# Kernel tuning notes

Hardware: AMD Instinct MI355X
Metric: run time of the kernel (lower is better)

The kernel has to match this reference:

```python
import jax, jax.numpy as jnp
import numpy as np
from jax import lax

B, P, ENC, H, A, E, V, TC = 64, 196, 2048, 1024, 1024, 512, 10000, 32


def setup_inputs() -> dict:
    key = jax.random.key(0)
    ks = jax.random.split(key, 24)
    s = 0.02
    inp = {
        'enc_out': jax.random.normal(ks[0], (B, P, ENC), jnp.float32),
        'enc_captions': jax.random.randint(ks[1], (B, TC), 0, V),
        'lengths': jax.random.randint(ks[2], (B,), 2, TC + 1).at[0].set(TC),
        'W_enc_att': jax.random.normal(ks[3], (A, ENC)) * s,
        'b_enc_att': jnp.zeros((A,)),
        'W_dec_att': jax.random.normal(ks[4], (A, H)) * s,
        'b_dec_att': jnp.zeros((A,)),
        'W_full': jax.random.normal(ks[5], (1, A)) * s,
        'b_full': jnp.zeros((1,)),
        'emb': jax.random.uniform(ks[6], (V, E), minval=-0.1, maxval=0.1),
        'W_ih': jax.random.normal(ks[7], (4 * H, E + ENC)) * s,
        'b_ih': jnp.zeros((4 * H,)),
        'W_hh': jax.random.normal(ks[8], (4 * H, H)) * s,
        'b_hh': jnp.zeros((4 * H,)),
        'W_init_h': jax.random.normal(ks[9], (H, ENC)) * s,
        'b_init_h': jnp.zeros((H,)),
        'W_init_c': jax.random.normal(ks[10], (H, ENC)) * s,
        'b_init_c': jnp.zeros((H,)),
        'W_beta': jax.random.normal(ks[11], (ENC, H)) * s,
        'b_beta': jnp.zeros((ENC,)),
        'W_fc': jax.random.uniform(ks[12], (V, H), minval=-0.1, maxval=0.1),
        'b_fc': jnp.zeros((V,)),
    }
    return inp


def reference(enc_out, enc_captions, lengths,
              W_enc_att, b_enc_att, W_dec_att, b_dec_att, W_full, b_full,
              emb, W_ih, b_ih, W_hh, b_hh,
              W_init_h, b_init_h, W_init_c, b_init_c,
              W_beta, b_beta, W_fc, b_fc):
    T = enc_captions.shape[1] - 1  # static max decode length (setup forces one full-length row)
    ind = jnp.argsort(-lengths)
    lens = lengths[ind]
    eo = enc_out[ind]              # [B,P,ENC] sorted by length desc
    caps = enc_captions[ind]
    dec_lens = lens - 1
    embs = emb[caps]               # [B,TC,E]

    mean_a = eo.mean(axis=1)
    h0 = mean_a @ W_init_h.T + b_init_h
    c0 = mean_a @ W_init_c.T + b_init_c

    # encoder projection is time-invariant; hoist out of the loop
    enc_att = jnp.einsum('bpe,ae->bpa', eo, W_enc_att) + b_enc_att  # [B,P,A]

    mask_ts = jnp.arange(T)[:, None] < dec_lens[None, :]            # [T,B]
    emb_ts = jnp.swapaxes(embs[:, :T, :], 0, 1)                     # [T,B,E]

    def step(carry, xs):
        h, c = carry
        emb_t, m = xs  # [B,E], [B] bool (active rows = leading batch_size_t)
        # attention
        dec = h @ W_dec_att.T + b_dec_att                            # [B,A]
        a = jax.nn.relu(enc_att + dec[:, None, :]) @ W_full[0] + b_full[0]  # [B,P]
        alpha = jax.nn.softmax(a, axis=1)
        context = jnp.einsum('bpe,bp->be', eo, alpha)                # [B,ENC]
        # gate + LSTM cell (torch gate order: i, f, g, o)
        gate = jax.nn.sigmoid(h @ W_beta.T + b_beta)
        awe = gate * context
        x = jnp.concatenate([emb_t, awe], axis=1)
        gates = x @ W_ih.T + b_ih + h @ W_hh.T + b_hh
        i, f, g, o = jnp.split(gates, 4, axis=1)
        c_new = jax.nn.sigmoid(f) * c + jax.nn.sigmoid(i) * jnp.tanh(g)
        h_new = jax.nn.sigmoid(o) * jnp.tanh(c_new)
        m2 = m[:, None]
        h2 = jnp.where(m2, h_new, h)  # inactive rows keep frozen state
        c2 = jnp.where(m2, c_new, c)
        mf = m2.astype(h.dtype)
        preds = (h_new @ W_fc.T + b_fc) * mf  # dropout = identity (eval)
        return (h2, c2), (preds, alpha * mf)

    (_, _), (preds, alphas) = lax.scan(step, (h0, c0), (emb_ts, mask_ts))
    predictions = jnp.swapaxes(preds, 0, 1)   # [B,T,V]
    alphas = jnp.swapaxes(alphas, 0, 1)       # [B,T,P]
    return predictions, alphas, caps, dec_lens, ind
```

## Files before the change

kernel.cpp:

```cpp
#include <hip/hip_runtime.h>

#define Bn   64
#define Pp   196
#define ENCd 2048
#define Hd   1024
#define Ad   1024
#define Ed   512
#define Vd   10000
#define TCd  32
#define Td   31
#define XHW  3584
#define VPAD 10240
#define KHL  6144

typedef short bf16x8 __attribute__((ext_vector_type(8)));
typedef float f32x4  __attribute__((ext_vector_type(4)));

static __device__ __forceinline__ float bf2f(unsigned short u) {
    unsigned int x = ((unsigned int)u) << 16;
    float f; __builtin_memcpy(&f, &x, 4); return f;
}
static __device__ __forceinline__ unsigned short f2bf(float f) {
    unsigned int x; __builtin_memcpy(&x, &f, 4);
    x += 0x7fffu + ((x >> 16) & 1u);
    return (unsigned short)(x >> 16);
}
static __device__ __forceinline__ float sigf(float x) { return 1.f / (1.f + expf(-x)); }

static __device__ __forceinline__ void gl_lds16(const unsigned short* g, unsigned short* l) {
    __builtin_amdgcn_global_load_lds((const __attribute__((address_space(1))) void*)g,
                                     (__attribute__((address_space(3))) void*)l,
                                     16, 0, 0);
}


__global__ void sort_kernel(const int* __restrict__ lengths, const int* __restrict__ captions,
                            int* __restrict__ ind, int* __restrict__ dl,
                            float* __restrict__ out_caps, float* __restrict__ out_dl,
                            float* __restrict__ out_ind) {
    __shared__ int s_ind[Bn];
    int tid = threadIdx.x;
    int Lt = lengths[tid];
    int pos = 0;
    for (int k = 0; k < Bn; ++k) {
        int Lk = lengths[k];
        pos += (Lk > Lt) || (Lk == Lt && k < tid);
    }
    s_ind[pos] = tid;
    __syncthreads();
    int src = s_ind[tid];
    ind[tid] = src;
    int d = lengths[src] - 1;
    dl[tid] = d;
    out_ind[tid] = (float)src;
    out_dl[tid] = (float)d;
    for (int j = 0; j < TCd; ++j)
        out_caps[tid * TCd + j] = (float)captions[src * TCd + j];
}

__global__ void cvt_kernel(const float* __restrict__ src, unsigned short* __restrict__ dst, int n) {
    int i = blockIdx.x * 256 + threadIdx.x;
    int stride = gridDim.x * 256;
    for (; i < n; i += stride) dst[i] = f2bf(src[i]);
}

__global__ void wcat_kernel(const float* __restrict__ wih, const float* __restrict__ whh,
                            unsigned short* __restrict__ wcat) {
    int j = blockIdx.y;
    int idx = blockIdx.x * 256 + threadIdx.x;
    float v = (idx < 2560) ? wih[(size_t)j * 2560 + idx] : whh[(size_t)j * 1024 + (idx - 2560)];
    wcat[(size_t)j * XHW + idx] = f2bf(v);
}

__global__ void biascat_kernel(const float* __restrict__ bih, const float* __restrict__ bhh,
                               float* __restrict__ bc) {
    int i = blockIdx.x * 256 + threadIdx.x;
    bc[i] = bih[i] + bhh[i];
}

__global__ void gather_eo_kernel(const float* __restrict__ enc_out, const int* __restrict__ ind,
                                 unsigned short* __restrict__ eo) {
    int b = blockIdx.y;
    int idx = blockIdx.x * 256 + threadIdx.x;
    int src = ind[b];
    eo[(size_t)b * (Pp * ENCd) + idx] = f2bf(enc_out[(size_t)src * (Pp * ENCd) + idx]);
}

__global__ void mean_kernel(const float* __restrict__ enc_out, const int* __restrict__ ind,
                            float* __restrict__ meanf) {
    int b = blockIdx.y;
    int e = blockIdx.x * 256 + threadIdx.x;
    int src = ind[b];
    const float* base = enc_out + (size_t)src * (Pp * ENCd) + e;
    float s = 0.f;
    for (int p = 0; p < Pp; ++p) s += base[(size_t)p * ENCd];
    meanf[b * ENCd + e] = s * (1.f / 196.f);
}

__global__ void embs_kernel(const float* __restrict__ emb, const int* __restrict__ captions,
                            const int* __restrict__ ind, unsigned short* __restrict__ xhbuf) {
    int b = blockIdx.y;
    int idx = blockIdx.x * 256 + threadIdx.x;
    int t = idx >> 9, e = idx & 511;
    int src = ind[b];
    int cap = captions[src * TCd + t];
    xhbuf[((size_t)t * Bn + b) * XHW + e] = f2bf(emb[(size_t)cap * Ed + e]);
}

__global__ void hilo_w_kernel(const float* __restrict__ winh, const float* __restrict__ winc,
                              unsigned short* __restrict__ dst) {
    int n = blockIdx.y;
    int k = blockIdx.x * 256 + threadIdx.x;
    const float* src = (n < 1024) ? (winh + (size_t)n * ENCd)
                                  : (winc + (size_t)(n - 1024) * ENCd);
    float v = src[k];
    unsigned short hi = f2bf(v);
    unsigned short lo = f2bf(v - bf2f(hi));
    size_t row = (size_t)n * KHL;
    dst[row + k]        = hi;
    dst[row + 2048 + k] = hi;
    dst[row + 4096 + k] = lo;
}

__global__ void hilo_a_kernel(const float* __restrict__ meanf, unsigned short* __restrict__ dst) {
    int id = blockIdx.x * 256 + threadIdx.x;
    int m = id >> 11, k = id & 2047;
    float v = meanf[id];
    unsigned short hi = f2bf(v);
    unsigned short lo = f2bf(v - bf2f(hi));
    size_t row = (size_t)m * KHL;
    dst[row + k]        = hi;
    dst[row + 2048 + k] = lo;
    dst[row + 4096 + k] = hi;
}

__global__ void initred_kernel(const float* __restrict__ part,
                               const float* __restrict__ binh, const float* __restrict__ binc,
                               unsigned short* __restrict__ xh0, float* __restrict__ cbuf) {
    int id = blockIdx.x * 256 + threadIdx.x;
    int m = id >> 11, n = id & 2047;
    bool is_c = n >= 1024;
    int nn = is_c ? n - 1024 : n;
    float acc = is_c ? binc[nn] : binh[nn];
#pragma unroll
    for (int s = 0; s < 8; ++s)
        acc += part[((size_t)(s * Bn + m)) * 2048 + n];
    if (is_c) cbuf[(size_t)m * Hd + nn] = acc;
    else      xh0[(size_t)m * XHW + 2560 + nn] = f2bf(acc);
}

template<int EPI>
__global__ __launch_bounds__(256)
void gemm_tile(const unsigned short* __restrict__ A, int lda,
               const unsigned short* __restrict__ W, int ldw,
               const float* __restrict__ bias,
               int N, int nbn, int K,
               float* __restrict__ outf, unsigned short* __restrict__ outb, int ldo,
               const int* __restrict__ dl) {
    __shared__ unsigned short lA[128 * 32];
    __shared__ unsigned short lB[128 * 32];

    int tid  = threadIdx.x;
    int wave = tid >> 6, lane = tid & 63;
    int mt = blockIdx.x / nbn;
    int nt = blockIdx.x % nbn;
    int m0 = mt * 128, n0 = nt * 128;

    int rs = lane >> 2;
    int cs = (lane & 3) * 8;
    const unsigned short* aG0 = A + (size_t)(m0 + wave * 16 + rs) * lda + cs;
    const unsigned short* aG1 = aG0 + (size_t)64 * lda;
    const unsigned short* bG0 = W + (size_t)(n0 + wave * 16 + rs) * ldw + cs;
    const unsigned short* bG1 = bG0 + (size_t)64 * ldw;
    unsigned short* lA0 = &lA[(wave * 16) * 32];
    unsigned short* lA1 = &lA[(64 + wave * 16) * 32];
    unsigned short* lB0 = &lB[(wave * 16) * 32];
    unsigned short* lB1 = &lB[(64 + wave * 16) * 32];

    int wr = wave >> 1, wc = wave & 1;
    int col = lane & 15, quad = lane >> 4;

    f32x4 acc[4][4];
#pragma unroll
    for (int i = 0; i < 4; ++i)
#pragma unroll
        for (int j = 0; j < 4; ++j) acc[i][j] = (f32x4){0.f, 0.f, 0.f, 0.f};

    for (int kt = 0; kt < K; kt += 32) {
        __syncthreads();
        gl_lds16(aG0 + kt, lA0);
        gl_lds16(aG1 + kt, lA1);
        gl_lds16(bG0 + kt, lB0);
        gl_lds16(bG1 + kt, lB1);
        __syncthreads();

        bf16x8 af[4], bf[4];
#pragma unroll
        for (int i = 0; i < 4; ++i) {
            af[i] = *(const bf16x8*)&lA[(wr * 64 + i * 16 + col) * 32 + quad * 8];
            bf[i] = *(const bf16x8*)&lB[(wc * 64 + i * 16 + col) * 32 + quad * 8];
        }
#pragma unroll
        for (int mi = 0; mi < 4; ++mi)
#pragma unroll
            for (int nj = 0; nj < 4; ++nj)
                acc[mi][nj] = __builtin_amdgcn_mfma_f32_16x16x32_bf16(af[mi], bf[nj], acc[mi][nj], 0, 0, 0);
    }

#pragma unroll
    for (int mi = 0; mi < 4; ++mi) {
#pragma unroll
        for (int r = 0; r < 4; ++r) {
            int m = m0 + wr * 64 + mi * 16 + quad * 4 + r;
            if (EPI == 5 && m >= Td * Bn) continue;
#pragma unroll
            for (int nj = 0; nj < 4; ++nj) {
                int n = n0 + wc * 64 + nj * 16 + col;
                if (EPI == 1) {
                    outb[(size_t)m * ldo + n] = f2bf(acc[mi][nj][r] + bias[n]);
                } else {
                    if (n < N) {
                        int t = m >> 6, b = m & 63;
                        float mf = (t < dl[b]) ? 1.f : 0.f;
                        float v = acc[mi][nj][r] + bias[n];
                        outf[((size_t)b * Td + t) * Vd + n] = v * mf;
                    }
                }
            }
        }
    }
}

template<int SK>
__global__ void gemm_sk4(const unsigned short* __restrict__ A, int lda,
                         const unsigned short* __restrict__ W,
                         int N, int K, float* __restrict__ part) {
    int wid  = (blockIdx.x * 256 + threadIdx.x) >> 6;
    int lane = threadIdx.x & 63;
    int ntiles = N >> 4;
    int s = wid / ntiles;
    int nt = wid - s * ntiles;
    int col = lane & 15, quad = lane >> 4;
    int kLen = K / SK, k0 = s * kLen;

    const unsigned short* aptr = A + (size_t)col * lda + k0 + quad * 8;
    const unsigned short* wptr = W + (size_t)(nt * 16 + col) * K + k0 + quad * 8;

    f32x4 acc[4];
#pragma unroll
    for (int i = 0; i < 4; ++i) acc[i] = (f32x4){0.f, 0.f, 0.f, 0.f};

    for (int k = 0; k < kLen; k += 32) {
        bf16x8 wf = *(const bf16x8*)(wptr + k);
#pragma unroll
        for (int mi = 0; mi < 4; ++mi) {
            bf16x8 af = *(const bf16x8*)(aptr + (size_t)mi * 16 * lda + k);
            acc[mi] = __builtin_amdgcn_mfma_f32_16x16x32_bf16(af, wf, acc[mi], 0, 0, 0);
        }
    }

    int n = nt * 16 + col;
    float* base = part + (size_t)s * Bn * N;
#pragma unroll
    for (int mi = 0; mi < 4; ++mi) {
#pragma unroll
        for (int r = 0; r < 4; ++r) {
            int m = mi * 16 + quad * 4 + r;
            base[(size_t)m * N + n] = acc[mi][r];
        }
    }
}


__global__ void scores_kernel(const float* __restrict__ pdb, const float* __restrict__ bdec,
                              const unsigned short* __restrict__ encatt,
                              const float* __restrict__ wfull,
                              float* __restrict__ scores) {
    int b = blockIdx.y;
    int tid = threadIdx.x;
    __shared__ float sdec[Ad];
    for (int i = tid; i < Ad; i += 256) {
        float v = bdec[i];
#pragma unroll
        for (int s2 = 0; s2 < 4; ++s2) v += pdb[((size_t)(s2 * Bn + b)) * 3072 + i];
        sdec[i] = v;
    }
    __syncthreads();
    int wave = tid >> 6, lane = tid & 63;
    int p = blockIdx.x * 4 + wave;
    const unsigned int* ea = (const unsigned int*)(encatt + ((size_t)(b * Pp + p) << 10));
    const float2* dp = (const float2*)sdec;
    const float2* wf = (const float2*)wfull;
    float acc = 0.f;
#pragma unroll
    for (int it = 0; it < 8; ++it) {
        int i2 = it * 64 + lane;
        unsigned int u = ea[i2];
        float2 dv = dp[i2];
        float2 wv = wf[i2];
        acc += fmaxf(bf2f((unsigned short)(u & 0xffffu)) + dv.x, 0.f) * wv.x;
        acc += fmaxf(bf2f((unsigned short)(u >> 16)) + dv.y, 0.f) * wv.y;
    }
    for (int o2 = 32; o2; o2 >>= 1) acc += __shfl_xor(acc, o2);
    if (lane == 0) scores[b * Pp + p] = acc;
}

__global__ void softmaxctx_kernel(const float* __restrict__ scores,
                                  const float* __restrict__ pdb, const float* __restrict__ bbeta,
                                  const unsigned short* __restrict__ eo,
                                  unsigned short* __restrict__ xh_t,
                                  float* __restrict__ out_alpha,
                                  const int* __restrict__ dl, int t) {
    int b = blockIdx.y, tid = threadIdx.x;
    __shared__ float red[256];
    __shared__ float sal[Pp];
    float s = (tid < Pp) ? scores[b * Pp + tid] : -1e30f;
    red[tid] = s; __syncthreads();
    for (int o2 = 128; o2; o2 >>= 1) { if (tid < o2) red[tid] = fmaxf(red[tid], red[tid + o2]); __syncthreads(); }
    float mx = red[0]; __syncthreads();
    float e = (tid < Pp) ? expf(s - mx) : 0.f;
    red[tid] = e; __syncthreads();
    for (int o2 = 128; o2; o2 >>= 1) { if (tid < o2) red[tid] += red[tid + o2]; __syncthreads(); }
    float inv = 1.f / red[0];
    if (tid < Pp) {
        float a = e * inv;
        sal[tid] = a;
        if (blockIdx.x == 0) {
            float mf = (t < dl[b]) ? 1.f : 0.f;
            out_alpha[((size_t)b * Td + t) * Pp + tid] = a * mf;
        }
    }
    __syncthreads();

    int e0 = blockIdx.x * 512 + tid * 2;
    const unsigned int* base = (const unsigned int*)(eo + (size_t)b * Pp * ENCd);
    int half = e0 >> 1;
    float a0 = 0.f, a1 = 0.f;
    for (int p = 0; p < Pp; ++p) {
        unsigned int u = base[p * (ENCd / 2) + half];
        float w = sal[p];
        a0 += w * bf2f((unsigned short)(u & 0xffffu));
        a1 += w * bf2f((unsigned short)(u >> 16));
    }
    float g0 = bbeta[e0], g1 = bbeta[e0 + 1];
#pragma unroll
    for (int s2 = 0; s2 < 4; ++s2) {
        const float* pb = pdb + ((size_t)(s2 * Bn + b)) * 3072 + Ad + e0;
        g0 += pb[0]; g1 += pb[1];
    }
    g0 = sigf(g0); g1 = sigf(g1);
    xh_t[(size_t)b * XHW + 512 + e0]     = f2bf(a0 * g0);
    xh_t[(size_t)b * XHW + 512 + e0 + 1] = f2bf(a1 * g1);
}

__global__ void lstm_kernel(const float* __restrict__ pg, const float* __restrict__ biascat,
                            float* __restrict__ c,
                            const unsigned short* __restrict__ xh_cur,
                            unsigned short* __restrict__ xh_next,
                            unsigned short* __restrict__ hall, const int* __restrict__ dl, int t) {
    int id = blockIdx.x * 256 + threadIdx.x;
    int b = id >> 10, j = id & 1023;
    float iv = biascat[j], fv = biascat[1024 + j], gv = biascat[2048 + j], ov = biascat[3072 + j];
#pragma unroll
    for (int s2 = 0; s2 < 8; ++s2) {
        const float* base = pg + ((size_t)(s2 * Bn + b)) * 4096;
        iv += base[j]; fv += base[1024 + j]; gv += base[2048 + j]; ov += base[3072 + j];
    }
    float co = c[id];
    float cn = sigf(fv) * co + sigf(iv) * tanhf(gv);
    float hn = sigf(ov) * tanhf(cn);
    bool m = t < dl[b];
    float ho = bf2f(xh_cur[(size_t)b * XHW + 2560 + j]);
    float h2 = m ? hn : ho;
    c[id] = m ? cn : co;
    xh_next[(size_t)b * XHW + 2560 + j] = f2bf(h2);
    hall[((size_t)t * Bn + b) * Hd + j] = f2bf(hn);
}


extern "C" void kernel_launch(void* const* d_in, const int* in_sizes, int n_in,
                              void* d_out, int out_size, void* d_ws, size_t ws_size,
                              hipStream_t stream) {
    const float* enc_out   = (const float*)d_in[0];
    const int*   captions  = (const int*)d_in[1];
    const int*   lengths   = (const int*)d_in[2];
    const float* W_enc_att = (const float*)d_in[3];
    const float* b_enc_att = (const float*)d_in[4];
    const float* W_dec_att = (const float*)d_in[5];
    const float* b_dec_att = (const float*)d_in[6];
    const float* W_full    = (const float*)d_in[7];
    const float* emb       = (const float*)d_in[9];
    const float* W_ih      = (const float*)d_in[10];
    const float* b_ih      = (const float*)d_in[11];
    const float* W_hh      = (const float*)d_in[12];
    const float* b_hh      = (const float*)d_in[13];
    const float* W_init_h  = (const float*)d_in[14];
    const float* b_init_h  = (const float*)d_in[15];
    const float* W_init_c  = (const float*)d_in[16];
    const float* b_init_c  = (const float*)d_in[17];
    const float* W_beta    = (const float*)d_in[18];
    const float* b_beta    = (const float*)d_in[19];
    const float* W_fc      = (const float*)d_in[20];
    const float* b_fc      = (const float*)d_in[21];

    float* out       = (float*)d_out;
    float* out_pred  = out;
    float* out_alpha = out + (size_t)Bn * Td * Vd;
    float* out_caps  = out_alpha + (size_t)Bn * Td * Pp;
    float* out_dl    = out_caps + (size_t)Bn * TCd;
    float* out_ind   = out_dl + Bn;

    char* ws = (char*)d_ws;
    size_t off = 0;
    auto take = [&](size_t n) -> char* {
        char* p = ws + off;
        off = (off + n + 255) & ~(size_t)255;
        return p;
    };
    int* ind_i   = (int*)take(Bn * 4);
    int* dl_i    = (int*)take(Bn * 4);
    unsigned short* eo_b     = (unsigned short*)take((size_t)Bn * Pp * ENCd * 2);
    unsigned short* encatt_b = (unsigned short*)take((size_t)Bn * Pp * Ad * 2);
    unsigned short* wcat_b   = (unsigned short*)take((size_t)4096 * XHW * 2);
    unsigned short* wfc_b    = (unsigned short*)take((size_t)VPAD * Hd * 2);
    unsigned short* wenc_b   = (unsigned short*)take((size_t)Ad * ENCd * 2);
    unsigned short* wdb_b    = (unsigned short*)take((size_t)3072 * Hd * 2);
    float*          biascat  = (float*)take(4096 * 4);
    float*          meanf    = (float*)take((size_t)Bn * ENCd * 4);
    unsigned short* xhbuf    = (unsigned short*)take((size_t)32 * Bn * XHW * 2);
    float*          cbuf     = (float*)take((size_t)Bn * Hd * 4);
    unsigned short* hall     = (unsigned short*)take((size_t)2048 * Hd * 2);
    float*          scores   = (float*)take((size_t)Bn * Pp * 4);
    float*          pdb      = (float*)take((size_t)4 * Bn * 3072 * 4);
    float*          pgates   = (float*)take((size_t)8 * Bn * 4096 * 4);
    unsigned short* ahl      = (unsigned short*)take((size_t)Bn * KHL * 2);
    unsigned short* whl   = encatt_b;
    float*          pinit = pgates;
    (void)ws_size; (void)out_size; (void)n_in; (void)in_sizes;

    sort_kernel<<<1, 64, 0, stream>>>(lengths, captions, ind_i, dl_i, out_caps, out_dl, out_ind);

    auto cvt = [&](const float* s, unsigned short* d, int n) {
        int g = (n + 255) / 256; if (g > 4096) g = 4096;
        cvt_kernel<<<g, 256, 0, stream>>>(s, d, n);
    };
    cvt(W_enc_att, wenc_b, Ad * ENCd);
    cvt(W_dec_att, wdb_b, Ad * Hd);
    cvt(W_beta,  wdb_b + (size_t)Ad * Hd, ENCd * Hd);
    cvt(W_fc,    wfc_b,   Vd * Hd);
    wcat_kernel<<<dim3(14, 4096), 256, 0, stream>>>(W_ih, W_hh, wcat_b);
    biascat_kernel<<<16, 256, 0, stream>>>(b_ih, b_hh, biascat);

    gather_eo_kernel<<<dim3(1568, Bn), 256, 0, stream>>>(enc_out, ind_i, eo_b);
    mean_kernel<<<dim3(8, Bn), 256, 0, stream>>>(enc_out, ind_i, meanf);
    embs_kernel<<<dim3(62, Bn), 256, 0, stream>>>(emb, captions, ind_i, xhbuf);

    hilo_w_kernel<<<dim3(8, 2048), 256, 0, stream>>>(W_init_h, W_init_c, whl);
    hilo_a_kernel<<<512, 256, 0, stream>>>(meanf, ahl);
    gemm_sk4<8><<<256, 256, 0, stream>>>(ahl, KHL, whl, 2048, KHL, pinit);
    initred_kernel<<<512, 256, 0, stream>>>(pinit, b_init_h, b_init_c, xhbuf, cbuf);

    gemm_tile<1><<<98 * 8, 256, 0, stream>>>(eo_b, ENCd, wenc_b, ENCd, b_enc_att,
        Ad, 8, ENCd, nullptr, encatt_b, Ad, nullptr);

    for (int t = 0; t < Td; ++t) {
        unsigned short* xh_t = xhbuf + (size_t)t * Bn * XHW;
        unsigned short* xh_n = xhbuf + (size_t)(t + 1) * Bn * XHW;

        gemm_sk4<4><<<192, 256, 0, stream>>>(xh_t + 2560, XHW, wdb_b, 3072, Hd, pdb);

        scores_kernel<<<dim3(49, Bn), 256, 0, stream>>>(pdb, b_dec_att, encatt_b, W_full, scores);

        softmaxctx_kernel<<<dim3(4, Bn), 256, 0, stream>>>(scores, pdb, b_beta, eo_b,
            xh_t, out_alpha, dl_i, t);

        gemm_sk4<8><<<512, 256, 0, stream>>>(xh_t, XHW, wcat_b, 4096, XHW, pgates);

        lstm_kernel<<<256, 256, 0, stream>>>(pgates, biascat, cbuf, xh_t, xh_n, hall, dl_i, t);
    }

    gemm_tile<5><<<16 * 80, 256, 0, stream>>>(hall, Hd, wfc_b, Hd, b_fc,
        Vd, 80, Hd, out_pred, nullptr, 0, dl_i);
}
```

Baseline: 2.322 ms.

## Fuse gather and mean, template split-K GEMM, widen dec split, use shuffle softmax

Merges the encoder gather/bf16 conversion and the spatial mean into one kernel that reads enc_out once using float4 loads. The mean is written as four partial sums that are combined in hilo_a. The split-K GEMM now takes its K chunk as a template constant with an unrolled loop. The per-step decoder/beta projection goes from 4 to 8 K-splits with twice as many blocks, and its consumers now sum 8 partials. The softmax reductions switch from LDS tree loops to wave shuffles, and the context loop is unrolled. The gather_mean launch has only 512 blocks, which may leave the GPU under-occupied for a large streaming pass.

```diff
diff --git a/kernel.cpp b/kernel.cpp
--- a/kernel.cpp
+++ b/kernel.cpp
@@ -15,6 +15,7 @@
 
 typedef short bf16x8 __attribute__((ext_vector_type(8)));
 typedef float f32x4  __attribute__((ext_vector_type(4)));
+typedef unsigned short u16x4 __attribute__((ext_vector_type(4)));
 
 static __device__ __forceinline__ float bf2f(unsigned short u) {
     unsigned int x = ((unsigned int)u) << 16;
@@ -78,23 +79,25 @@
     bc[i] = bih[i] + bhh[i];
 }
 
-__global__ void gather_eo_kernel(const float* __restrict__ enc_out, const int* __restrict__ ind,
-                                 unsigned short* __restrict__ eo) {
+__global__ void gather_mean_kernel(const float* __restrict__ enc_out, const int* __restrict__ ind,
+                                   unsigned short* __restrict__ eo, float* __restrict__ psum) {
     int b = blockIdx.y;
-    int idx = blockIdx.x * 256 + threadIdx.x;
+    int bx = blockIdx.x;
+    int pc = bx >> 1, eh = bx & 1;
+    int e = eh * 1024 + threadIdx.x * 4;
     int src = ind[b];
-    eo[(size_t)b * (Pp * ENCd) + idx] = f2bf(enc_out[(size_t)src * (Pp * ENCd) + idx]);
-}
-
-__global__ void mean_kernel(const float* __restrict__ enc_out, const int* __restrict__ ind,
-                            float* __restrict__ meanf) {
-    int b = blockIdx.y;
-    int e = blockIdx.x * 256 + threadIdx.x;
-    int src = ind[b];
-    const float* base = enc_out + (size_t)src * (Pp * ENCd) + e;
-    float s = 0.f;
-    for (int p = 0; p < Pp; ++p) s += base[(size_t)p * ENCd];
-    meanf[b * ENCd + e] = s * (1.f / 196.f);
+    const float4* base = (const float4*)(enc_out + (size_t)src * (Pp * ENCd));
+    unsigned short* eob = eo + (size_t)b * (Pp * ENCd);
+    float ax = 0.f, ay = 0.f, az = 0.f, aw = 0.f;
+    int p0 = pc * 49;
+    for (int p = p0; p < p0 + 49; ++p) {
+        float4 v = base[p * (ENCd / 4) + (e >> 2)];
+        ax += v.x; ay += v.y; az += v.z; aw += v.w;
+        u16x4 w; w[0] = f2bf(v.x); w[1] = f2bf(v.y); w[2] = f2bf(v.z); w[3] = f2bf(v.w);
+        *(u16x4*)(eob + (size_t)p * ENCd + e) = w;
+    }
+    float4 s4; s4.x = ax; s4.y = ay; s4.z = az; s4.w = aw;
+    *(float4*)(psum + ((size_t)(pc * Bn + b)) * ENCd + e) = s4;
 }
 
 __global__ void embs_kernel(const float* __restrict__ emb, const int* __restrict__ captions,
@@ -122,10 +125,13 @@
     dst[row + 4096 + k] = lo;
 }
 
-__global__ void hilo_a_kernel(const float* __restrict__ meanf, unsigned short* __restrict__ dst) {
+__global__ void hilo_a_kernel(const float* __restrict__ psum, unsigned short* __restrict__ dst) {
     int id = blockIdx.x * 256 + threadIdx.x;
     int m = id >> 11, k = id & 2047;
-    float v = meanf[id];
+    float v = (psum[((size_t)(0 * Bn + m)) * ENCd + k] +
+               psum[((size_t)(1 * Bn + m)) * ENCd + k] +
+               psum[((size_t)(2 * Bn + m)) * ENCd + k] +
+               psum[((size_t)(3 * Bn + m)) * ENCd + k]) * (1.f / 196.f);
     unsigned short hi = f2bf(v);
     unsigned short lo = f2bf(v - bf2f(hi));
     size_t row = (size_t)m * KHL;
@@ -231,17 +237,18 @@
     }
 }
 
-template<int SK>
+template<int SK, int KCH>
 __global__ void gemm_sk4(const unsigned short* __restrict__ A, int lda,
                          const unsigned short* __restrict__ W,
-                         int N, int K, float* __restrict__ part) {
+                         int N, float* __restrict__ part) {
+    const int K = SK * KCH;
     int wid  = (blockIdx.x * 256 + threadIdx.x) >> 6;
     int lane = threadIdx.x & 63;
     int ntiles = N >> 4;
     int s = wid / ntiles;
     int nt = wid - s * ntiles;
     int col = lane & 15, quad = lane >> 4;
-    int kLen = K / SK, k0 = s * kLen;
+    int k0 = s * KCH;
 
     const unsigned short* aptr = A + (size_t)col * lda + k0 + quad * 8;
     const unsigned short* wptr = W + (size_t)(nt * 16 + col) * K + k0 + quad * 8;
@@ -250,7 +257,8 @@
 #pragma unroll
     for (int i = 0; i < 4; ++i) acc[i] = (f32x4){0.f, 0.f, 0.f, 0.f};
 
-    for (int k = 0; k < kLen; k += 32) {
+#pragma unroll 4
+    for (int k = 0; k < KCH; k += 32) {
         bf16x8 wf = *(const bf16x8*)(wptr + k);
 #pragma unroll
         for (int mi = 0; mi < 4; ++mi) {
@@ -282,7 +290,7 @@
     for (int i = tid; i < Ad; i += 256) {
         float v = bdec[i];
 #pragma unroll
-        for (int s2 = 0; s2 < 4; ++s2) v += pdb[((size_t)(s2 * Bn + b)) * 3072 + i];
+        for (int s2 = 0; s2 < 8; ++s2) v += pdb[((size_t)(s2 * Bn + b)) * 3072 + i];
         sdec[i] = v;
     }
     __syncthreads();
@@ -312,16 +320,21 @@
                                   float* __restrict__ out_alpha,
                                   const int* __restrict__ dl, int t) {
     int b = blockIdx.y, tid = threadIdx.x;
-    __shared__ float red[256];
+    int wave = tid >> 6, lane = tid & 63;
+    __shared__ float red4[8];
     __shared__ float sal[Pp];
     float s = (tid < Pp) ? scores[b * Pp + tid] : -1e30f;
-    red[tid] = s; __syncthreads();
-    for (int o2 = 128; o2; o2 >>= 1) { if (tid < o2) red[tid] = fmaxf(red[tid], red[tid + o2]); __syncthreads(); }
-    float mx = red[0]; __syncthreads();
+    float wm = s;
+    for (int o2 = 32; o2; o2 >>= 1) wm = fmaxf(wm, __shfl_xor(wm, o2));
+    if (lane == 0) red4[wave] = wm;
+    __syncthreads();
+    float mx = fmaxf(fmaxf(red4[0], red4[1]), fmaxf(red4[2], red4[3]));
     float e = (tid < Pp) ? expf(s - mx) : 0.f;
-    red[tid] = e; __syncthreads();
-    for (int o2 = 128; o2; o2 >>= 1) { if (tid < o2) red[tid] += red[tid + o2]; __syncthreads(); }
-    float inv = 1.f / red[0];
+    float ws = e;
+    for (int o2 = 32; o2; o2 >>= 1) ws += __shfl_xor(ws, o2);
+    if (lane == 0) red4[4 + wave] = ws;
+    __syncthreads();
+    float inv = 1.f / (red4[4] + red4[5] + red4[6] + red4[7]);
     if (tid < Pp) {
         float a = e * inv;
         sal[tid] = a;
@@ -336,6 +349,7 @@
     const unsigned int* base = (const unsigned int*)(eo + (size_t)b * Pp * ENCd);
     int half = e0 >> 1;
     float a0 = 0.f, a1 = 0.f;
+#pragma unroll 4
     for (int p = 0; p < Pp; ++p) {
         unsigned int u = base[p * (ENCd / 2) + half];
         float w = sal[p];
@@ -344,7 +358,7 @@
     }
     float g0 = bbeta[e0], g1 = bbeta[e0 + 1];
 #pragma unroll
-    for (int s2 = 0; s2 < 4; ++s2) {
+    for (int s2 = 0; s2 < 8; ++s2) {
         const float* pb = pdb + ((size_t)(s2 * Bn + b)) * 3072 + Ad + e0;
         g0 += pb[0]; g1 += pb[1];
     }
@@ -426,12 +440,12 @@
     unsigned short* wenc_b   = (unsigned short*)take((size_t)Ad * ENCd * 2);
     unsigned short* wdb_b    = (unsigned short*)take((size_t)3072 * Hd * 2);
     float*          biascat  = (float*)take(4096 * 4);
-    float*          meanf    = (float*)take((size_t)Bn * ENCd * 4);
+    float*          psum     = (float*)take((size_t)4 * Bn * ENCd * 4);
     unsigned short* xhbuf    = (unsigned short*)take((size_t)32 * Bn * XHW * 2);
     float*          cbuf     = (float*)take((size_t)Bn * Hd * 4);
     unsigned short* hall     = (unsigned short*)take((size_t)2048 * Hd * 2);
     float*          scores   = (float*)take((size_t)Bn * Pp * 4);
-    float*          pdb      = (float*)take((size_t)4 * Bn * 3072 * 4);
+    float*          pdb      = (float*)take((size_t)8 * Bn * 3072 * 4);
     float*          pgates   = (float*)take((size_t)8 * Bn * 4096 * 4);
     unsigned short* ahl      = (unsigned short*)take((size_t)Bn * KHL * 2);
     unsigned short* whl   = encatt_b;
@@ -451,13 +465,12 @@
     wcat_kernel<<<dim3(14, 4096), 256, 0, stream>>>(W_ih, W_hh, wcat_b);
     biascat_kernel<<<16, 256, 0, stream>>>(b_ih, b_hh, biascat);
 
-    gather_eo_kernel<<<dim3(1568, Bn), 256, 0, stream>>>(enc_out, ind_i, eo_b);
-    mean_kernel<<<dim3(8, Bn), 256, 0, stream>>>(enc_out, ind_i, meanf);
+    gather_mean_kernel<<<dim3(8, Bn), 256, 0, stream>>>(enc_out, ind_i, eo_b, psum);
     embs_kernel<<<dim3(62, Bn), 256, 0, stream>>>(emb, captions, ind_i, xhbuf);
 
     hilo_w_kernel<<<dim3(8, 2048), 256, 0, stream>>>(W_init_h, W_init_c, whl);
-    hilo_a_kernel<<<512, 256, 0, stream>>>(meanf, ahl);
-    gemm_sk4<8><<<256, 256, 0, stream>>>(ahl, KHL, whl, 2048, KHL, pinit);
+    hilo_a_kernel<<<512, 256, 0, stream>>>(psum, ahl);
+    gemm_sk4<8, 768><<<256, 256, 0, stream>>>(ahl, KHL, whl, 2048, pinit);
     initred_kernel<<<512, 256, 0, stream>>>(pinit, b_init_h, b_init_c, xhbuf, cbuf);
 
     gemm_tile<1><<<98 * 8, 256, 0, stream>>>(eo_b, ENCd, wenc_b, ENCd, b_enc_att,
@@ -467,14 +480,14 @@
         unsigned short* xh_t = xhbuf + (size_t)t * Bn * XHW;
         unsigned short* xh_n = xhbuf + (size_t)(t + 1) * Bn * XHW;
 
-        gemm_sk4<4><<<192, 256, 0, stream>>>(xh_t + 2560, XHW, wdb_b, 3072, Hd, pdb);
+        gemm_sk4<8, 128><<<384, 256, 0, stream>>>(xh_t + 2560, XHW, wdb_b, 3072, pdb);
 
         scores_kernel<<<dim3(49, Bn), 256, 0, stream>>>(pdb, b_dec_att, encatt_b, W_full, scores);
 
         softmaxctx_kernel<<<dim3(4, Bn), 256, 0, stream>>>(scores, pdb, b_beta, eo_b,
             xh_t, out_alpha, dl_i, t);
 
-        gemm_sk4<8><<<512, 256, 0, stream>>>(xh_t, XHW, wcat_b, 4096, XHW, pgates);
+        gemm_sk4<8, 448><<<512, 256, 0, stream>>>(xh_t, XHW, wcat_b, 4096, pgates);
 
         lstm_kernel<<<256, 256, 0, stream>>>(pgates, biascat, cbuf, xh_t, xh_n, hall, dl_i, t);
     }
```

Result: slower. 2.507 ms (+8.0%).
